# Performance work log

Hardware: AMD Instinct MI355X
Metric: run time of the kernel (lower is better)

Reference implementation:

```python
import jax, jax.numpy as jnp
import numpy as np

A, NA, D_OBS, B = 16, 8, 64, 128  # agents, actions, obs dim, graphs
DZ = D_OBS + NA  # obs_z_input_dim = 72


def _mlp(x, W1, b1, W2, b2):
    # Linear -> leaky_relu(0.01) -> Linear, torch Linear convention (y = x @ W.T + b)
    return jax.nn.leaky_relu(x @ W1.T + b1) @ W2.T + b2


def setup_inputs() -> dict:
    key = jax.random.key(0)
    ks = iter(jax.random.split(key, 40))
    p = {}
    p["obs"] = jax.random.normal(next(ks), (B * A, D_OBS), jnp.float32)
    p["policies"] = jax.random.uniform(next(ks), (B * A, NA), jnp.float32)
    p["actions"] = jax.random.uniform(next(ks), (B * A, NA), jnp.float32)

    def mk(name, inp, out):
        p[name + "_w"] = jax.random.normal(next(ks), (out, inp), jnp.float32) / np.sqrt(inp).astype(np.float32)
        p[name + "_b"] = jax.random.normal(next(ks), (out,), jnp.float32) * 0.01

    mk("kw1", D_OBS, 64); mk("kw2", 64, 64)   # key_weight layers
    mk("qw1", D_OBS, 64); mk("qw2", 64, 64)   # query_weight layers
    mk("ko1", DZ, 64);    mk("ko2", 64, 64)   # key_obsz layers
    mk("qo1", DZ, 64);    mk("qo2", 64, 64)   # query_obsz layers
    mk("av1", DZ, 64);    mk("av2", 64, 64)   # attention_value_obsz layers
    mk("fv1", 128, 64);   mk("fv2", 64, 8)    # final_value layers
    return p


def reference(obs, policies, actions,
              kw1_w, kw1_b, kw2_w, kw2_b, qw1_w, qw1_b, qw2_w, qw2_b,
              ko1_w, ko1_b, ko2_w, ko2_b, qo1_w, qo1_b, qo2_w, qo2_b,
              av1_w, av1_b, av2_w, av2_b, fv1_w, fv1_b, fv2_w, fv2_b):
    d_k_w = jnp.sqrt(jnp.float32(kw2_w.shape[0]))
    d_k_o = jnp.sqrt(jnp.float32(ko2_w.shape[0]))
    Bn = obs.shape[0] // A
    obs_b = obs.reshape(Bn, A, -1)                      # [B,A,Dobs]
    pi = policies.reshape(Bn, A, NA)
    act = actions.reshape(Bn, A, NA)

    # --- DGL update_all on the fully-connected (with self-loop) per-batch graph ---
    key_z = _mlp(obs_b, kw1_w, kw1_b, kw2_w, kw2_b)     # [B,A,dk]
    query_z = _mlp(obs_b, qw1_w, qw1_b, qw2_w, qw2_b)
    score = jnp.einsum('bjd,bid->bij', key_z, query_z)  # src key j -> dst query i
    w = jax.nn.sigmoid(score / d_k_w)[..., None]        # [B,A,A,1], mailbox gate
    z = w * act[:, None] + (1.0 - w) * pi[:, None]      # [B,A(i),A(j),NA]
    weight_z = w.reshape(Bn * A, A, 1)

    # obs_z[b,i,j] = cat(obs[b,j], z[b,i,j])
    obs_rep = jnp.broadcast_to(obs_b[:, None], (Bn, A, A, obs_b.shape[-1]))
    obs_z = jnp.concatenate([obs_rep, z], axis=-1)      # [B,A,A,DZ]

    diag = jnp.arange(A)
    src = obs_z[:, diag, diag]                          # source_obs_z_: [B,A,DZ] (j==i entry)

    key_o = _mlp(src, ko1_w, ko1_b, ko2_w, ko2_b)       # broadcast over j
    query_o = _mlp(obs_z, qo1_w, qo1_b, qo2_w, qo2_b)   # [B,A,A,dk]
    score_o = jnp.einsum('bid,bijd->bij', key_o, query_o)
    weights_o = jax.nn.softmax(jnp.exp(jnp.clip(score_o / d_k_o, -5.0, 5.0)), axis=-1)  # [B,A,A]

    # obs_z_pi[b,i,j,k] = op[b,j] if k==j else obs_z[b,i,k], op = cat(obs, pi)
    op = jnp.concatenate([obs_b, pi], axis=-1)          # [B,A,DZ]
    m = jnp.eye(A, dtype=obs.dtype)[None, None, :, :, None]          # (j,k) mask
    obs_z_pi = obs_z[:, :, None] * (1.0 - m) + op[:, None, None] * m  # [B,A,A,A,DZ]

    attn_src = _mlp(src, av1_w, av1_b, av2_w, av2_b)                  # [B,A,O]
    attn_other = _mlp(obs_z_pi, av1_w, av1_b, av2_w, av2_b)           # [B,A,A,A,O]

    w_exp = weights_o[:, None, :, :, None]              # [b,i,j,k,1] = weights_o[b,j,k]
    mixed = jnp.mean(attn_other * w_exp, axis=-2)       # mean over k -> [B,A,A,O]
    src_rep = jnp.broadcast_to(attn_src[:, None], mixed.shape)
    node_features = jnp.concatenate([src_rep, mixed], axis=-1)        # [B,A,A,2O]
    value = _mlp(node_features, fv1_w, fv1_b, fv2_w, fv2_b)           # [B,A,A,8]

    weights_obsz = jnp.broadcast_to(w_exp, (Bn, A, A, A, 1))
    return value, weight_z, weights_obsz
```

## Files before the change

kernel.cpp:

```cpp
#include <hip/hip_runtime.h>

#define A_ 16
#define NA_ 8
#define DOBS_ 64

typedef _Float16 f16;
typedef f16 h2 __attribute__((ext_vector_type(2)));
typedef f16 v8h __attribute__((ext_vector_type(8)));
typedef float v4f __attribute__((ext_vector_type(4)));

__device__ __forceinline__ float fdot2f(h2 a, h2 b, float c) {
  return __builtin_amdgcn_fdot2(a, b, c, false);
}
__device__ __forceinline__ float lrelu(float x) { return x > 0.f ? x : 0.01f * x; }

__device__ __forceinline__ float dot64(const float* w, const float* x) {
  float a0 = 0.f, a1 = 0.f, a2 = 0.f, a3 = 0.f;
#pragma unroll
  for (int d = 0; d < 64; d += 4) {
    const float4 wv = *(const float4*)(w + d);
    const float4 xv = *(const float4*)(x + d);
    a0 += wv.x * xv.x; a1 += wv.y * xv.y; a2 += wv.z * xv.z; a3 += wv.w * xv.w;
  }
  return (a0 + a1) + (a2 + a3);
}

struct P {
  const float *obs, *pol, *act;
  const float *kw1w, *kw1b, *kw2w, *kw2b, *qw1w, *qw1b, *qw2w, *qw2b;
  const float *ko1w, *ko1b, *ko2w, *ko2b, *qo1w, *qo1b, *qo2w, *qo2b;
  const float *av1w, *av1b, *av2w, *av2b, *fv1w, *fv1b, *fv2w, *fv2b;
  float *out0, *out1, *out2;
  float *wsig, *wo;
};


struct alignas(16) SMem1 {
  float obs[16][68];
  float pi[16][8], act[16][8];
  float wsig[16][16];
  float wo[16][16];
  float c0[16];
  float GF2[16 * 16 * 4];
  float wz8n[16 * 32];
  float ht[16][68];
  float a1[16][68];
  float a2[16][68];
  struct { float w[64 * 68]; float b[64]; float z[64 * 8]; } W;
};

__device__ __forceinline__ void mini256(const float* W, const float* bias, int addbias,
                                        const float (*X)[68], float (*Y)[68], int relu, int tid) {
  if (tid < 256) {
    const int r = tid >> 4, ob = tid & 15;
    float acc[4];
#pragma unroll
    for (int oo = 0; oo < 4; oo++) acc[oo] = addbias ? bias[ob + 16 * oo] : 0.f;
    for (int d = 0; d < 64; d += 4) {
      const float4 xv = *(const float4*)(&X[r][d]);
#pragma unroll
      for (int oo = 0; oo < 4; oo++) {
        const float4 wv = *(const float4*)(W + (ob + 16 * oo) * 68 + d);
        acc[oo] += wv.x * xv.x + wv.y * xv.y + wv.z * xv.z + wv.w * xv.w;
      }
    }
#pragma unroll
    for (int oo = 0; oo < 4; oo++) {
      float v = acc[oo];
      if (relu) v = lrelu(v);
      Y[r][ob + 16 * oo] = v;
    }
  }
}

__device__ __forceinline__ void stage68(float* dst, const float* src, int tid) {
  for (int k = tid; k < 4096; k += 1024) dst[(k >> 6) * 68 + (k & 63)] = src[k];
}

__global__ __launch_bounds__(1024) void critic_k1(P p) {
  __shared__ SMem1 s;
  const int tid = threadIdx.x;
  const int b = blockIdx.x;

  for (int k = tid; k < 1024; k += 1024) s.obs[k >> 6][k & 63] = p.obs[(size_t)b * 1024 + k];
  if (tid < 128) s.pi[tid >> 3][tid & 7] = p.pol[(size_t)b * 128 + tid];
  else if (tid < 256) { int k = tid - 128; s.act[k >> 3][k & 7] = p.act[(size_t)b * 128 + k]; }
  stage68(s.W.w, p.kw1w, tid);
  if (tid < 64) s.W.b[tid] = p.kw1b[tid];
  __syncthreads();
  mini256(s.W.w, s.W.b, 1, s.obs, s.ht, 1, tid);
  __syncthreads();
  stage68(s.W.w, p.kw2w, tid);
  if (tid < 64) s.W.b[tid] = p.kw2b[tid];
  __syncthreads();
  mini256(s.W.w, s.W.b, 1, s.ht, s.a1, 0, tid);
  __syncthreads();
  stage68(s.W.w, p.qw1w, tid);
  if (tid < 64) s.W.b[tid] = p.qw1b[tid];
  __syncthreads();
  mini256(s.W.w, s.W.b, 1, s.obs, s.ht, 1, tid);
  __syncthreads();
  stage68(s.W.w, p.qw2w, tid);
  if (tid < 64) s.W.b[tid] = p.qw2b[tid];
  __syncthreads();
  mini256(s.W.w, s.W.b, 1, s.ht, s.a2, 0, tid);
  __syncthreads();

  if (tid < 256) {
    const int i = tid >> 4, j = tid & 15;
    const float sc = dot64(&s.a2[i][0], &s.a1[j][0]);
    const float w = 1.f / (1.f + __expf(-sc * 0.125f));
    s.wsig[i][j] = w;
    p.out1[(size_t)b * 256 + tid] = w;
    p.wsig[(size_t)b * 256 + tid] = w;
  }
  for (int k = tid; k < 4096; k += 1024) { int o = k >> 6, c = k & 63; s.W.w[o * 68 + c] = p.ko1w[o * 72 + c]; }
  for (int k = tid; k < 512; k += 1024) { int o = k >> 3, c = k & 7; s.W.z[o * 8 + c] = p.ko1w[o * 72 + 64 + c]; }
  if (tid < 64) s.W.b[tid] = p.ko1b[tid];
  __syncthreads();

  if (tid < 256) {
    const int r = tid >> 4, ob = tid & 15;
    const float wrr = s.wsig[r][r];
    float z[8];
#pragma unroll
    for (int c = 0; c < 8; c++) z[c] = s.pi[r][c] + wrr * (s.act[r][c] - s.pi[r][c]);
#pragma unroll
    for (int oo = 0; oo < 4; oo++) {
      const int o = ob + 16 * oo;
      float a = s.W.b[o] + dot64(s.W.w + o * 68, &s.obs[r][0]);
#pragma unroll
      for (int c = 0; c < 8; c++) a += s.W.z[o * 8 + c] * z[c];
      s.ht[r][o] = lrelu(a);
    }
  }
  __syncthreads();
  stage68(s.W.w, p.ko2w, tid);
  if (tid < 64) s.W.b[tid] = p.ko2b[tid];
  __syncthreads();
  mini256(s.W.w, s.W.b, 1, s.ht, s.a2, 0, tid);
  __syncthreads();

  for (int k = tid; k < 4096; k += 1024) { int o2 = k >> 6, o = k & 63; s.W.w[o * 68 + o2] = p.qo2w[k]; }
  if (tid < 64) s.W.b[tid] = p.qo2b[tid];
  __syncthreads();
  mini256(s.W.w, s.W.b, 0, s.a2, s.a1, 0, tid);
  if (tid < 16) {
    float c = 0.f;
    for (int d = 0; d < 64; d++) c += s.a2[tid][d] * s.W.b[d];
    s.c0[tid] = c;
  }
  __syncthreads();

  for (int k = tid; k < 4096; k += 1024) { int o = k >> 6, c = k & 63; s.W.w[o * 68 + c] = p.qo1w[o * 72 + c]; }
  for (int k = tid; k < 512; k += 1024) { int o = k >> 3, c = k & 7; s.wz8n[(o & 15) * 32 + (o >> 4) * 8 + c] = p.qo1w[o * 72 + 64 + c]; }
  if (tid < 64) s.W.b[tid] = p.qo1b[tid];
  __syncthreads();
  if (tid < 256) {
    const int j = tid >> 4, ob = tid & 15;
#pragma unroll
    for (int oo = 0; oo < 4; oo++) {
      const int o = ob + 16 * oo;
      s.GF2[ob * 64 + j * 4 + oo] = dot64(s.W.w + o * 68, &s.obs[j][0]) + s.W.b[o];
    }
  }
  __syncthreads();

  {
    const int q = tid >> 2, g = tid & 3;
    const int qi = q >> 4, qj = q & 15;
    const float wij = s.wsig[qi][qj];
    float z[8];
#pragma unroll
    for (int c = 0; c < 8; c++) z[c] = s.pi[qj][c] + wij * (s.act[qj][c] - s.pi[qj][c]);
    float sc = 0.f;
#pragma unroll
    for (int t = 0; t < 16; t++) {
      const float4 wa = *(const float4*)(&s.wz8n[t * 32 + g * 8]);
      const float4 wb = *(const float4*)(&s.wz8n[t * 32 + g * 8 + 4]);
      float hv = s.GF2[t * 64 + qj * 4 + g]
        + wa.x * z[0] + wa.y * z[1] + wa.z * z[2] + wa.w * z[3]
        + wb.x * z[4] + wb.y * z[5] + wb.z * z[6] + wb.w * z[7];
      hv = lrelu(hv);
      sc += s.a1[qi][g * 16 + t] * hv;
    }
    sc += __shfl_xor(sc, 1);
    sc += __shfl_xor(sc, 2);
    if (g == 0) {
      float yv = (sc + s.c0[qi]) * 0.125f;
      yv = fminf(fmaxf(yv, -5.f), 5.f);
      ((float*)s.ht)[qi * 16 + qj] = __expf(yv);
    }
  }
  __syncthreads();

  if (tid < 256) {
    const int i = tid >> 4, j = tid & 15;
    const float* e = (const float*)s.ht;
    float m = -1e30f;
#pragma unroll
    for (int jj = 0; jj < 16; jj++) m = fmaxf(m, e[i * 16 + jj]);
    float den = 0.f;
#pragma unroll
    for (int jj = 0; jj < 16; jj++) den += __expf(e[i * 16 + jj] - m);
    const float val = __expf(e[i * 16 + j] - m) / den;
    s.wo[i][j] = val;
    p.wo[(size_t)b * 256 + tid] = val;
  }
  __syncthreads();

  {
    const int q = tid >> 2, g = tid & 3, k = q & 15;
    *(float4*)(p.out2 + ((size_t)b * 256 + q) * 16 + 4 * g) =
        make_float4(s.wo[k][4 * g], s.wo[k][4 * g + 1], s.wo[k][4 * g + 2], s.wo[k][4 * g + 3]);
  }
}


struct alignas(16) SMem2 {
  f16 obsH[16][72];
  f16 AOsrcD[16 * 72];
  f16 APT[64 * 24];
  f16 AextH[16 * 40];
  f16 fv2pw[8 * 64];
  f16 slice[8][1536];
  union {
    struct { f16 av1H[64 * 96]; f16 av2H[64 * 72]; } av;
    f16 fv1H[64 * 136];
  } W;
  float pi[16][8], act[16][8], wsig[16][16];
  float av1b[64], av2b[64], fv1b[64], fv2b[8];
};

__device__ __forceinline__ v8h bfrag(const f16* Wm, int stride, int nt, int ks, int lane) {
  const int n = lane & 15, q = lane >> 4;
  return *(const v8h*)(Wm + (nt * 16 + n) * stride + ks * 32 + q * 8);
}

__device__ __forceinline__ void av_mlp(const SMem2& s, f16* Hbuf, v8h az, int lane, v4f acc2[4]) {
  const int m = lane & 15, q = lane >> 4;
  const v8h a0 = *(const v8h*)(&s.obsH[m][q * 8]);
  const v8h a1 = *(const v8h*)(&s.obsH[m][32 + q * 8]);
#pragma unroll
  for (int nt = 0; nt < 4; nt++) {
    const float bv = s.av1b[nt * 16 + m];
    v4f acc = {bv, bv, bv, bv};
    acc = __builtin_amdgcn_mfma_f32_16x16x32_f16(a0, bfrag(s.W.av.av1H, 96, nt, 0, lane), acc, 0, 0, 0);
    acc = __builtin_amdgcn_mfma_f32_16x16x32_f16(a1, bfrag(s.W.av.av1H, 96, nt, 1, lane), acc, 0, 0, 0);
    acc = __builtin_amdgcn_mfma_f32_16x16x32_f16(az, bfrag(s.W.av.av1H, 96, nt, 2, lane), acc, 0, 0, 0);
#pragma unroll
    for (int reg = 0; reg < 4; reg++)
      Hbuf[(q * 4 + reg) * 72 + nt * 16 + m] = (f16)lrelu(acc[reg]);
  }
  const v8h h0 = *(const v8h*)(Hbuf + m * 72 + q * 8);
  const v8h h1 = *(const v8h*)(Hbuf + m * 72 + 32 + q * 8);
#pragma unroll
  for (int nt = 0; nt < 4; nt++) {
    const float bv = s.av2b[nt * 16 + m];
    v4f acc = {bv, bv, bv, bv};
    acc = __builtin_amdgcn_mfma_f32_16x16x32_f16(h0, bfrag(s.W.av.av2H, 72, nt, 0, lane), acc, 0, 0, 0);
    acc = __builtin_amdgcn_mfma_f32_16x16x32_f16(h1, bfrag(s.W.av.av2H, 72, nt, 1, lane), acc, 0, 0, 0);
    acc2[nt] = acc;
  }
}

__global__ __launch_bounds__(512) void critic_k2(P p) {
  __shared__ SMem2 s;
  const int tid = threadIdx.x;
  const int b = blockIdx.x >> 1, ibase = (blockIdx.x & 1) * 8;
  const int w = tid >> 6, lane = tid & 63;
  const int m = lane & 15, quad = lane >> 4;
  const int i = ibase + w;

  for (int k = tid; k < 1024; k += 512) s.obsH[k >> 6][k & 63] = (f16)p.obs[(size_t)b * 1024 + k];
  if (tid < 128) { s.pi[tid >> 3][tid & 7] = p.pol[(size_t)b * 128 + tid]; }
  else if (tid < 256) { int k = tid - 128; s.act[k >> 3][k & 7] = p.act[(size_t)b * 128 + k]; }
  for (int k = tid; k < 256; k += 512) s.wsig[k >> 4][k & 15] = p.wsig[(size_t)b * 256 + k];
  {
    const int kk = tid >> 5, j2 = tid & 31;
    float v = 0.f;
    if (j2 < 16) v = p.wo[(size_t)b * 256 + kk * 16 + j2] * 0.0625f;
    else if (j2 - 16 == kk) v = p.wo[(size_t)b * 256 + kk * 16 + kk] * 0.0625f;
    s.AextH[kk * 40 + j2] = (f16)v;
  }
  for (int k = tid; k < 4608; k += 512) { int r = k / 72, c = k - r * 72; s.W.av.av1H[r * 96 + c] = (f16)p.av1w[k]; }
  for (int k = tid; k < 64 * 24; k += 512) { int r = k / 24, c = 72 + (k - r * 24); s.W.av.av1H[r * 96 + c] = (f16)0.f; }
  for (int k = tid; k < 4096; k += 512) s.W.av.av2H[(k >> 6) * 72 + (k & 63)] = (f16)p.av2w[k];
  for (int k = tid; k < 512; k += 512) s.fv2pw[k] = (f16)p.fv2w[k];
  if (tid < 64) { s.av1b[tid] = p.av1b[tid]; s.av2b[tid] = p.av2b[tid]; s.fv1b[tid] = p.fv1b[tid]; }
  else if (tid < 72) s.fv2b[tid - 64] = p.fv2b[tid - 64];
  __syncthreads();

  f16* Sl = &s.slice[w][0];
  {
    v8h az = {};
    if (quad == 0) {
      const float wv = s.wsig[i][m];
#pragma unroll
      for (int c = 0; c < 8; c++) az[c] = (f16)(s.pi[m][c] + wv * (s.act[m][c] - s.pi[m][c]));
    }
    v4f acc2[4];
    av_mlp(s, Sl, az, lane, acc2);
#pragma unroll
    for (int nt = 0; nt < 4; nt++)
#pragma unroll
      for (int reg = 0; reg < 4; reg++)
        Sl[(nt * 16 + m) * 24 + quad * 4 + reg] = (f16)acc2[nt][reg];
  }
  if (w == 0) {
    v8h az = {};
    if (quad == 0) {
#pragma unroll
      for (int c = 0; c < 8; c++) az[c] = (f16)s.pi[m][c];
    }
    v4f acc2[4];
    av_mlp(s, s.APT, az, lane, acc2);
#pragma unroll
    for (int nt = 0; nt < 4; nt++)
#pragma unroll
      for (int reg = 0; reg < 4; reg++)
        s.APT[(nt * 16 + m) * 24 + quad * 4 + reg] = (f16)acc2[nt][reg];
  }
  if (w == 1) {
    v8h az = {};
    if (quad == 0) {
      const float wv = s.wsig[m][m];
#pragma unroll
      for (int c = 0; c < 8; c++) az[c] = (f16)(s.pi[m][c] + wv * (s.act[m][c] - s.pi[m][c]));
    }
    v4f acc2[4];
    av_mlp(s, s.AOsrcD, az, lane, acc2);
#pragma unroll
    for (int nt = 0; nt < 4; nt++)
#pragma unroll
      for (int reg = 0; reg < 4; reg++)
        s.AOsrcD[(quad * 4 + reg) * 72 + nt * 16 + m] = (f16)acc2[nt][reg];
  }
  __syncthreads();

  for (int k = tid; k < 8192; k += 512) s.W.fv1H[(k >> 7) * 136 + (k & 127)] = (f16)p.fv1w[k];
  __syncthreads();

  {
    const v8h am = *(const v8h*)(&s.AextH[m * 40 + quad * 8]);
    v4f macc[4];
#pragma unroll
    for (int nt = 0; nt < 4; nt++) {
      const int o = nt * 16 + m;
      v8h bf;
      if (quad < 2) {
        bf = *(const v8h*)(Sl + o * 24 + quad * 8);
      } else {
        const v8h apv = *(const v8h*)(&s.APT[o * 24 + (quad - 2) * 8]);
        const v8h aov = *(const v8h*)(Sl + o * 24 + (quad - 2) * 8);
        bf = apv - aov;
      }
      v4f z4 = {0.f, 0.f, 0.f, 0.f};
      macc[nt] = __builtin_amdgcn_mfma_f32_16x16x32_f16(am, bf, z4, 0, 0, 0);
    }
#pragma unroll
    for (int nt = 0; nt < 4; nt++)
#pragma unroll
      for (int reg = 0; reg < 4; reg++)
        Sl[(quad * 4 + reg) * 72 + nt * 16 + m] = (f16)macc[nt][reg];
  }

  {
    const v8h f0 = *(const v8h*)(&s.AOsrcD[m * 72 + quad * 8]);
    const v8h f1 = *(const v8h*)(&s.AOsrcD[m * 72 + 32 + quad * 8]);
    const v8h f2 = *(const v8h*)(Sl + m * 72 + quad * 8);
    const v8h f3 = *(const v8h*)(Sl + m * 72 + 32 + quad * 8);
#pragma unroll
    for (int nt = 0; nt < 4; nt++) {
      const float bv = s.fv1b[nt * 16 + m];
      v4f acc = {bv, bv, bv, bv};
      acc = __builtin_amdgcn_mfma_f32_16x16x32_f16(f0, bfrag(s.W.fv1H, 136, nt, 0, lane), acc, 0, 0, 0);
      acc = __builtin_amdgcn_mfma_f32_16x16x32_f16(f1, bfrag(s.W.fv1H, 136, nt, 1, lane), acc, 0, 0, 0);
      acc = __builtin_amdgcn_mfma_f32_16x16x32_f16(f2, bfrag(s.W.fv1H, 136, nt, 2, lane), acc, 0, 0, 0);
      acc = __builtin_amdgcn_mfma_f32_16x16x32_f16(f3, bfrag(s.W.fv1H, 136, nt, 3, lane), acc, 0, 0, 0);
#pragma unroll
      for (int reg = 0; reg < 4; reg++)
        Sl[(quad * 4 + reg) * 72 + nt * 16 + m] = (f16)lrelu(acc[reg]);
    }
  }
  {
    const int g2 = quad;
    float y0 = s.fv2b[2 * g2], y1 = s.fv2b[2 * g2 + 1];
#pragma unroll
    for (int o2 = 0; o2 < 32; o2++) {
      const h2 hh = *(const h2*)(Sl + m * 72 + 2 * o2);
      const h2 w0 = *(const h2*)(&s.fv2pw[(2 * g2) * 64 + 2 * o2]);
      const h2 w1 = *(const h2*)(&s.fv2pw[(2 * g2 + 1) * 64 + 2 * o2]);
      y0 = fdot2f(w0, hh, y0);
      y1 = fdot2f(w1, hh, y1);
    }
    *(float2*)(p.out0 + ((size_t)b * 256 + i * 16 + m) * 8 + 2 * g2) = make_float2(y0, y1);
  }
}

extern "C" void kernel_launch(void* const* d_in, const int* in_sizes, int n_in,
                              void* d_out, int out_size, void* d_ws, size_t ws_size,
                              hipStream_t stream) {
  P p;
  p.obs = (const float*)d_in[0];
  p.pol = (const float*)d_in[1];
  p.act = (const float*)d_in[2];
  p.kw1w = (const float*)d_in[3];  p.kw1b = (const float*)d_in[4];
  p.kw2w = (const float*)d_in[5];  p.kw2b = (const float*)d_in[6];
  p.qw1w = (const float*)d_in[7];  p.qw1b = (const float*)d_in[8];
  p.qw2w = (const float*)d_in[9];  p.qw2b = (const float*)d_in[10];
  p.ko1w = (const float*)d_in[11]; p.ko1b = (const float*)d_in[12];
  p.ko2w = (const float*)d_in[13]; p.ko2b = (const float*)d_in[14];
  p.qo1w = (const float*)d_in[15]; p.qo1b = (const float*)d_in[16];
  p.qo2w = (const float*)d_in[17]; p.qo2b = (const float*)d_in[18];
  p.av1w = (const float*)d_in[19]; p.av1b = (const float*)d_in[20];
  p.av2w = (const float*)d_in[21]; p.av2b = (const float*)d_in[22];
  p.fv1w = (const float*)d_in[23]; p.fv1b = (const float*)d_in[24];
  p.fv2w = (const float*)d_in[25]; p.fv2b = (const float*)d_in[26];

  const int Bn = in_sizes[0] / (A_ * DOBS_);
  p.out0 = (float*)d_out;
  p.out1 = p.out0 + (size_t)Bn * A_ * A_ * NA_;
  p.out2 = p.out1 + (size_t)Bn * A_ * A_;
  p.wsig = (float*)d_ws;
  p.wo = p.wsig + (size_t)Bn * 256;

  hipLaunchKernelGGL(critic_k1, dim3(Bn), dim3(1024), 0, stream, p);
  hipLaunchKernelGGL(critic_k2, dim3(2 * Bn), dim3(512), 0, stream, p);
}
```

Before: 144.7 us.

## Prefetch all k1 weights into registers and run each layer on all 1024 threads

```diff
diff --git a/kernel.cpp b/kernel.cpp
--- a/kernel.cpp
+++ b/kernel.cpp
@@ -13,17 +13,6 @@
   return __builtin_amdgcn_fdot2(a, b, c, false);
 }
 __device__ __forceinline__ float lrelu(float x) { return x > 0.f ? x : 0.01f * x; }
-
-__device__ __forceinline__ float dot64(const float* w, const float* x) {
-  float a0 = 0.f, a1 = 0.f, a2 = 0.f, a3 = 0.f;
-#pragma unroll
-  for (int d = 0; d < 64; d += 4) {
-    const float4 wv = *(const float4*)(w + d);
-    const float4 xv = *(const float4*)(x + d);
-    a0 += wv.x * xv.x; a1 += wv.y * xv.y; a2 += wv.z * xv.z; a3 += wv.w * xv.w;
-  }
-  return (a0 + a1) + (a2 + a3);
-}
 
 struct P {
   const float *obs, *pol, *act;
@@ -35,168 +24,167 @@
 };
 
 
-struct alignas(16) SMem1 {
-  float obs[16][68];
-  float pi[16][8], act[16][8];
-  float wsig[16][16];
-  float wo[16][16];
-  float c0[16];
-  float GF2[16 * 16 * 4];
-  float wz8n[16 * 32];
-  float ht[16][68];
-  float a1[16][68];
-  float a2[16][68];
-  struct { float w[64 * 68]; float b[64]; float z[64 * 8]; } W;
-};
-
-__device__ __forceinline__ void mini256(const float* W, const float* bias, int addbias,
-                                        const float (*X)[68], float (*Y)[68], int relu, int tid) {
-  if (tid < 256) {
-    const int r = tid >> 4, ob = tid & 15;
-    float acc[4];
-#pragma unroll
-    for (int oo = 0; oo < 4; oo++) acc[oo] = addbias ? bias[ob + 16 * oo] : 0.f;
-    for (int d = 0; d < 64; d += 4) {
-      const float4 xv = *(const float4*)(&X[r][d]);
-#pragma unroll
-      for (int oo = 0; oo < 4; oo++) {
-        const float4 wv = *(const float4*)(W + (ob + 16 * oo) * 68 + d);
-        acc[oo] += wv.x * xv.x + wv.y * xv.y + wv.z * xv.z + wv.w * xv.w;
-      }
-    }
-#pragma unroll
-    for (int oo = 0; oo < 4; oo++) {
-      float v = acc[oo];
-      if (relu) v = lrelu(v);
-      Y[r][ob + 16 * oo] = v;
-    }
-  }
-}
-
-__device__ __forceinline__ void stage68(float* dst, const float* src, int tid) {
-  for (int k = tid; k < 4096; k += 1024) dst[(k >> 6) * 68 + (k & 63)] = src[k];
+#define SM_WQ0 0
+#define SM_WQ1 4096
+#define SM_S0 8192
+#define SM_S1 9280
+#define SM_S2 10368
+#define SM_S3 11456
+#define SM_OBS 12544
+#define SM_GF2 13632
+#define SM_WZ8 14656
+#define SM_WSIG 15168
+#define SM_WO 15424
+#define SM_PI 15680
+#define SM_ACT 15808
+#define SM_C0 15936
+#define SM_TOT 15952
+
+__device__ __forceinline__ float dotWq(const float* Wq, const float* xrow, int o) {
+  float a0 = 0.f, a1 = 0.f, a2 = 0.f, a3 = 0.f;
+#pragma unroll
+  for (int d4 = 0; d4 < 16; d4++) {
+    const float4 w = ((const float4*)Wq)[d4 * 64 + o];
+    const float4 x = *(const float4*)(xrow + 4 * d4);
+    a0 += w.x * x.x; a1 += w.y * x.y; a2 += w.z * x.z; a3 += w.w * x.w;
+  }
+  return (a0 + a1) + (a2 + a3);
 }
 
 __global__ __launch_bounds__(1024) void critic_k1(P p) {
-  __shared__ SMem1 s;
+  __shared__ float sm[SM_TOT];
   const int tid = threadIdx.x;
   const int b = blockIdx.x;
-
-  for (int k = tid; k < 1024; k += 1024) s.obs[k >> 6][k & 63] = p.obs[(size_t)b * 1024 + k];
-  if (tid < 128) s.pi[tid >> 3][tid & 7] = p.pol[(size_t)b * 128 + tid];
-  else if (tid < 256) { int k = tid - 128; s.act[k >> 3][k & 7] = p.act[(size_t)b * 128 + k]; }
-  stage68(s.W.w, p.kw1w, tid);
-  if (tid < 64) s.W.b[tid] = p.kw1b[tid];
-  __syncthreads();
-  mini256(s.W.w, s.W.b, 1, s.obs, s.ht, 1, tid);
-  __syncthreads();
-  stage68(s.W.w, p.kw2w, tid);
-  if (tid < 64) s.W.b[tid] = p.kw2b[tid];
-  __syncthreads();
-  mini256(s.W.w, s.W.b, 1, s.ht, s.a1, 0, tid);
-  __syncthreads();
-  stage68(s.W.w, p.qw1w, tid);
-  if (tid < 64) s.W.b[tid] = p.qw1b[tid];
-  __syncthreads();
-  mini256(s.W.w, s.W.b, 1, s.obs, s.ht, 1, tid);
-  __syncthreads();
-  stage68(s.W.w, p.qw2w, tid);
-  if (tid < 64) s.W.b[tid] = p.qw2b[tid];
-  __syncthreads();
-  mini256(s.W.w, s.W.b, 1, s.ht, s.a2, 0, tid);
-  __syncthreads();
-
-  if (tid < 256) {
-    const int i = tid >> 4, j = tid & 15;
-    const float sc = dot64(&s.a2[i][0], &s.a1[j][0]);
-    const float w = 1.f / (1.f + __expf(-sc * 0.125f));
-    s.wsig[i][j] = w;
-    p.out1[(size_t)b * 256 + tid] = w;
-    p.wsig[(size_t)b * 256 + tid] = w;
-  }
-  for (int k = tid; k < 4096; k += 1024) { int o = k >> 6, c = k & 63; s.W.w[o * 68 + c] = p.ko1w[o * 72 + c]; }
-  for (int k = tid; k < 512; k += 1024) { int o = k >> 3, c = k & 7; s.W.z[o * 8 + c] = p.ko1w[o * 72 + 64 + c]; }
-  if (tid < 64) s.W.b[tid] = p.ko1b[tid];
-  __syncthreads();
-
-  if (tid < 256) {
-    const int r = tid >> 4, ob = tid & 15;
-    const float wrr = s.wsig[r][r];
+  const int o = tid & 63, r = tid >> 6;
+
+  const float4 Rkw1 = *(const float4*)(p.kw1w + o * 64 + 4 * r);
+  const float4 Rqw1 = *(const float4*)(p.qw1w + o * 64 + 4 * r);
+  const float4 Rkw2 = *(const float4*)(p.kw2w + o * 64 + 4 * r);
+  const float4 Rqw2 = *(const float4*)(p.qw2w + o * 64 + 4 * r);
+  const float4 Rko2 = *(const float4*)(p.ko2w + o * 64 + 4 * r);
+  const float4 Rko1 = *(const float4*)(p.ko1w + o * 72 + 4 * r);
+  const float4 Rqo1 = *(const float4*)(p.qo1w + o * 72 + 4 * r);
+  const float4 Rkz0 = *(const float4*)(p.ko1w + o * 72 + 64);
+  const float4 Rkz1 = *(const float4*)(p.ko1w + o * 72 + 68);
+  float4 Rqo2;
+  Rqo2.x = p.qo2w[(4 * r + 0) * 64 + o];
+  Rqo2.y = p.qo2w[(4 * r + 1) * 64 + o];
+  Rqo2.z = p.qo2w[(4 * r + 2) * 64 + o];
+  Rqo2.w = p.qo2w[(4 * r + 3) * 64 + o];
+  const float Bkw1 = p.kw1b[o], Bkw2 = p.kw2b[o], Bqw1 = p.qw1b[o], Bqw2 = p.qw2b[o];
+  const float Bko1 = p.ko1b[o], Bko2 = p.ko2b[o], Bqo1 = p.qo1b[o], Bqo2v = p.qo2b[o];
+
+  sm[SM_OBS + r * 68 + o] = p.obs[(size_t)b * 1024 + tid];
+  if (tid < 128) sm[SM_PI + tid] = p.pol[(size_t)b * 128 + tid];
+  else if (tid < 256) sm[SM_ACT + tid - 128] = p.act[(size_t)b * 128 + tid - 128];
+  if (tid < 512) {
+    const int oo = tid >> 3, c = tid & 7;
+    sm[SM_WZ8 + (oo & 15) * 32 + (oo >> 4) * 8 + c] = p.qo1w[oo * 72 + 64 + c];
+  }
+  ((float4*)(sm + SM_WQ0))[tid] = Rkw1;
+  ((float4*)(sm + SM_WQ1))[tid] = Rqw1;
+  __syncthreads();
+
+  {
+    const float* xr = sm + SM_OBS + r * 68;
+    sm[SM_S0 + r * 68 + o] = lrelu(dotWq(sm + SM_WQ0, xr, o) + Bkw1);
+    sm[SM_S1 + r * 68 + o] = lrelu(dotWq(sm + SM_WQ1, xr, o) + Bqw1);
+  }
+  __syncthreads();
+  ((float4*)(sm + SM_WQ0))[tid] = Rkw2;
+  ((float4*)(sm + SM_WQ1))[tid] = Rqw2;
+  __syncthreads();
+
+  sm[SM_S2 + r * 68 + o] = dotWq(sm + SM_WQ0, sm + SM_S0 + r * 68, o) + Bkw2;
+  sm[SM_S3 + r * 68 + o] = dotWq(sm + SM_WQ1, sm + SM_S1 + r * 68, o) + Bqw2;
+  __syncthreads();
+  ((float4*)(sm + SM_WQ0))[tid] = Rqo1;
+  ((float4*)(sm + SM_WQ1))[tid] = Rko1;
+  __syncthreads();
+
+  {
+    const float gv = dotWq(sm + SM_WQ0, sm + SM_OBS + r * 68, o) + Bqo1;
+    sm[SM_GF2 + (o & 15) * 64 + r * 4 + (o >> 4)] = gv;
+    const int j = (tid >> 2) & 15, g = tid & 3;
+    float a0 = 0.f, a1 = 0.f, a2 = 0.f, a3 = 0.f;
+#pragma unroll
+    for (int t4 = 0; t4 < 4; t4++) {
+      const float4 qv = *(const float4*)(sm + SM_S3 + r * 68 + g * 16 + 4 * t4);
+      const float4 kv = *(const float4*)(sm + SM_S2 + j * 68 + g * 16 + 4 * t4);
+      a0 += qv.x * kv.x; a1 += qv.y * kv.y; a2 += qv.z * kv.z; a3 += qv.w * kv.w;
+    }
+    float sc = (a0 + a1) + (a2 + a3);
+    sc += __shfl_xor(sc, 1);
+    sc += __shfl_xor(sc, 2);
+    if (g == 0) {
+      const float w = 1.f / (1.f + __expf(-sc * 0.125f));
+      sm[SM_WSIG + r * 16 + j] = w;
+      p.out1[(size_t)b * 256 + r * 16 + j] = w;
+      p.wsig[(size_t)b * 256 + r * 16 + j] = w;
+    }
+  }
+  __syncthreads();
+
+  {
+    float acc = dotWq(sm + SM_WQ1, sm + SM_OBS + r * 68, o) + Bko1;
+    const float wrr = sm[SM_WSIG + r * 16 + r];
+    const float* piR = sm + SM_PI + r * 8;
+    const float* acR = sm + SM_ACT + r * 8;
     float z[8];
 #pragma unroll
-    for (int c = 0; c < 8; c++) z[c] = s.pi[r][c] + wrr * (s.act[r][c] - s.pi[r][c]);
-#pragma unroll
-    for (int oo = 0; oo < 4; oo++) {
-      const int o = ob + 16 * oo;
-      float a = s.W.b[o] + dot64(s.W.w + o * 68, &s.obs[r][0]);
-#pragma unroll
-      for (int c = 0; c < 8; c++) a += s.W.z[o * 8 + c] * z[c];
-      s.ht[r][o] = lrelu(a);
-    }
-  }
-  __syncthreads();
-  stage68(s.W.w, p.ko2w, tid);
-  if (tid < 64) s.W.b[tid] = p.ko2b[tid];
-  __syncthreads();
-  mini256(s.W.w, s.W.b, 1, s.ht, s.a2, 0, tid);
-  __syncthreads();
-
-  for (int k = tid; k < 4096; k += 1024) { int o2 = k >> 6, o = k & 63; s.W.w[o * 68 + o2] = p.qo2w[k]; }
-  if (tid < 64) s.W.b[tid] = p.qo2b[tid];
-  __syncthreads();
-  mini256(s.W.w, s.W.b, 0, s.a2, s.a1, 0, tid);
-  if (tid < 16) {
-    float c = 0.f;
-    for (int d = 0; d < 64; d++) c += s.a2[tid][d] * s.W.b[d];
-    s.c0[tid] = c;
-  }
-  __syncthreads();
-
-  for (int k = tid; k < 4096; k += 1024) { int o = k >> 6, c = k & 63; s.W.w[o * 68 + c] = p.qo1w[o * 72 + c]; }
-  for (int k = tid; k < 512; k += 1024) { int o = k >> 3, c = k & 7; s.wz8n[(o & 15) * 32 + (o >> 4) * 8 + c] = p.qo1w[o * 72 + 64 + c]; }
-  if (tid < 64) s.W.b[tid] = p.qo1b[tid];
-  __syncthreads();
-  if (tid < 256) {
-    const int j = tid >> 4, ob = tid & 15;
-#pragma unroll
-    for (int oo = 0; oo < 4; oo++) {
-      const int o = ob + 16 * oo;
-      s.GF2[ob * 64 + j * 4 + oo] = dot64(s.W.w + o * 68, &s.obs[j][0]) + s.W.b[o];
-    }
-  }
-  __syncthreads();
-
-  {
-    const int q = tid >> 2, g = tid & 3;
-    const int qi = q >> 4, qj = q & 15;
-    const float wij = s.wsig[qi][qj];
+    for (int c = 0; c < 8; c++) z[c] = piR[c] + wrr * (acR[c] - piR[c]);
+    acc += Rkz0.x * z[0] + Rkz0.y * z[1] + Rkz0.z * z[2] + Rkz0.w * z[3]
+         + Rkz1.x * z[4] + Rkz1.y * z[5] + Rkz1.z * z[6] + Rkz1.w * z[7];
+    sm[SM_S0 + r * 68 + o] = lrelu(acc);
+    ((float4*)(sm + SM_WQ0))[tid] = Rko2;
+  }
+  __syncthreads();
+
+  sm[SM_S1 + r * 68 + o] = dotWq(sm + SM_WQ0, sm + SM_S0 + r * 68, o) + Bko2;
+  ((float4*)(sm + SM_WQ1))[tid] = Rqo2;
+  __syncthreads();
+
+  {
+    sm[SM_S2 + r * 68 + o] = dotWq(sm + SM_WQ1, sm + SM_S1 + r * 68, o);
+    float t = sm[SM_S1 + r * 68 + o] * Bqo2v;
+#pragma unroll
+    for (int mm = 1; mm < 64; mm <<= 1) t += __shfl_xor(t, mm);
+    if (o == 0) sm[SM_C0 + r] = t;
+  }
+  __syncthreads();
+
+  {
+    const int j = (tid >> 2) & 15, g = tid & 3;
+    const float wij = sm[SM_WSIG + r * 16 + j];
+    const float* piR = sm + SM_PI + j * 8;
+    const float* acR = sm + SM_ACT + j * 8;
     float z[8];
 #pragma unroll
-    for (int c = 0; c < 8; c++) z[c] = s.pi[qj][c] + wij * (s.act[qj][c] - s.pi[qj][c]);
+    for (int c = 0; c < 8; c++) z[c] = piR[c] + wij * (acR[c] - piR[c]);
     float sc = 0.f;
 #pragma unroll
     for (int t = 0; t < 16; t++) {
-      const float4 wa = *(const float4*)(&s.wz8n[t * 32 + g * 8]);
-      const float4 wb = *(const float4*)(&s.wz8n[t * 32 + g * 8 + 4]);
-      float hv = s.GF2[t * 64 + qj * 4 + g]
+      const float4 wa = *(const float4*)(sm + SM_WZ8 + t * 32 + g * 8);
+      const float4 wb = *(const float4*)(sm + SM_WZ8 + t * 32 + g * 8 + 4);
+      float hv = sm[SM_GF2 + t * 64 + j * 4 + g]
         + wa.x * z[0] + wa.y * z[1] + wa.z * z[2] + wa.w * z[3]
         + wb.x * z[4] + wb.y * z[5] + wb.z * z[6] + wb.w * z[7];
       hv = lrelu(hv);
-      sc += s.a1[qi][g * 16 + t] * hv;
+      sc += sm[SM_S2 + r * 68 + g * 16 + t] * hv;
     }
     sc += __shfl_xor(sc, 1);
     sc += __shfl_xor(sc, 2);
     if (g == 0) {
-      float yv = (sc + s.c0[qi]) * 0.125f;
+      float yv = (sc + sm[SM_C0 + r]) * 0.125f;
       yv = fminf(fmaxf(yv, -5.f), 5.f);
-      ((float*)s.ht)[qi * 16 + qj] = __expf(yv);
+      sm[SM_S3 + r * 16 + j] = __expf(yv);
     }
   }
   __syncthreads();
 
   if (tid < 256) {
     const int i = tid >> 4, j = tid & 15;
-    const float* e = (const float*)s.ht;
+    const float* e = sm + SM_S3;
     float m = -1e30f;
 #pragma unroll
     for (int jj = 0; jj < 16; jj++) m = fmaxf(m, e[i * 16 + jj]);
@@ -204,15 +192,14 @@
 #pragma unroll
     for (int jj = 0; jj < 16; jj++) den += __expf(e[i * 16 + jj] - m);
     const float val = __expf(e[i * 16 + j] - m) / den;
-    s.wo[i][j] = val;
+    sm[SM_WO + i * 16 + j] = val;
     p.wo[(size_t)b * 256 + tid] = val;
   }
   __syncthreads();
-
   {
     const int q = tid >> 2, g = tid & 3, k = q & 15;
     *(float4*)(p.out2 + ((size_t)b * 256 + q) * 16 + 4 * g) =
-        make_float4(s.wo[k][4 * g], s.wo[k][4 * g + 1], s.wo[k][4 * g + 2], s.wo[k][4 * g + 3]);
+        *(const float4*)(sm + SM_WO + k * 16 + 4 * g);
   }
 }
 
@@ -272,6 +259,10 @@
   const int m = lane & 15, quad = lane >> 4;
   const int i = ibase + w;
 
+  float4 rfv[4];
+#pragma unroll
+  for (int qq = 0; qq < 4; qq++) rfv[qq] = ((const float4*)p.fv1w)[tid * 4 + qq];
+
   for (int k = tid; k < 1024; k += 512) s.obsH[k >> 6][k & 63] = (f16)p.obs[(size_t)b * 1024 + k];
   if (tid < 128) { s.pi[tid >> 3][tid & 7] = p.pol[(size_t)b * 128 + tid]; }
   else if (tid < 256) { int k = tid - 128; s.act[k >> 3][k & 7] = p.act[(size_t)b * 128 + k]; }
@@ -283,10 +274,18 @@
     else if (j2 - 16 == kk) v = p.wo[(size_t)b * 256 + kk * 16 + kk] * 0.0625f;
     s.AextH[kk * 40 + j2] = (f16)v;
   }
-  for (int k = tid; k < 4608; k += 512) { int r = k / 72, c = k - r * 72; s.W.av.av1H[r * 96 + c] = (f16)p.av1w[k]; }
-  for (int k = tid; k < 64 * 24; k += 512) { int r = k / 24, c = 72 + (k - r * 24); s.W.av.av1H[r * 96 + c] = (f16)0.f; }
+  {
+    const int row = tid >> 3, c0 = (tid & 7) * 9;
+#pragma unroll
+    for (int c = 0; c < 9; c++) s.W.av.av1H[row * 96 + c0 + c] = (f16)p.av1w[row * 72 + c0 + c];
+  }
+  {
+    const int row = tid >> 3, c0 = 72 + (tid & 7) * 3;
+#pragma unroll
+    for (int c = 0; c < 3; c++) s.W.av.av1H[row * 96 + c0 + c] = (f16)0.f;
+  }
   for (int k = tid; k < 4096; k += 512) s.W.av.av2H[(k >> 6) * 72 + (k & 63)] = (f16)p.av2w[k];
-  for (int k = tid; k < 512; k += 512) s.fv2pw[k] = (f16)p.fv2w[k];
+  s.fv2pw[tid] = (f16)p.fv2w[tid];
   if (tid < 64) { s.av1b[tid] = p.av1b[tid]; s.av2b[tid] = p.av2b[tid]; s.fv1b[tid] = p.fv1b[tid]; }
   else if (tid < 72) s.fv2b[tid - 64] = p.fv2b[tid - 64];
   __syncthreads();
@@ -338,7 +337,13 @@
   }
   __syncthreads();
 
-  for (int k = tid; k < 8192; k += 512) s.W.fv1H[(k >> 7) * 136 + (k & 127)] = (f16)p.fv1w[k];
+#pragma unroll
+  for (int qq = 0; qq < 4; qq++) {
+    const int e0 = tid * 16 + qq * 4;
+    h2* d = (h2*)&s.W.fv1H[(e0 >> 7) * 136 + (e0 & 127)];
+    d[0] = h2{(f16)rfv[qq].x, (f16)rfv[qq].y};
+    d[1] = h2{(f16)rfv[qq].z, (f16)rfv[qq].w};
+  }
   __syncthreads();
 
   {
```

Result: faster. 134.8 us (-6.9%).
